# Performance work log

Hardware: AMD Instinct MI355X
Metric: run time of the kernel (lower is better)

Reference implementation:

```python
import jax, jax.numpy as jnp
import numpy as np

# ---- config (mirrors init_kwargs) ----
T = 1024          # num tokens (one causal sequence)
H = 1024          # hidden_size
NQ, NK, D = 16, 4, 64   # q heads, kv heads, head_dim (GQA)
I_DENSE = 4096    # dense FFN intermediate
I_MOE = 512       # expert FFN intermediate
E, K = 8, 2       # num_experts, top_k
EPS = 1e-6
THETA = 10000.0


def setup_inputs() -> dict:
    key = jax.random.key(0)
    ks = jax.random.split(key, 20)
    rn = lambda k, shp: (jax.random.normal(k, shp, dtype=jnp.float32) * 0.02)
    QKV = (NQ + 2 * NK) * D
    return {
        "hidden_states": jax.random.normal(ks[0], (T, H), dtype=jnp.float32),
        "residual": jax.random.normal(ks[1], (T, H), dtype=jnp.float32),
        "positions": jnp.arange(T, dtype=jnp.int32),
        "ln0_w": jnp.ones((H,), jnp.float32),
        "pa0_w": jnp.ones((H,), jnp.float32),
        "ln1_w": jnp.ones((H,), jnp.float32),
        "pa1_w": jnp.ones((H,), jnp.float32),
        # attention weights (stored [in, out] so x @ W)
        "qkv0_w": rn(ks[2], (H, QKV)),
        "o0_w": rn(ks[3], (NQ * D, H)),
        "qkv1_w": rn(ks[4], (H, QKV)),
        "o1_w": rn(ks[5], (NQ * D, H)),
        # dense MLPs (merged gate_up: first half gate, second half up)
        "gu0_w": rn(ks[6], (H, 2 * I_DENSE)),
        "dn0_w": rn(ks[7], (I_DENSE, H)),
        "gu1_w": rn(ks[8], (H, 2 * I_DENSE)),
        "dn1_w": rn(ks[9], (I_DENSE, H)),
        # MoE: router gate + per-expert SwiGLU weights
        "gate_w": rn(ks[10], (H, E)),
        "w13": rn(ks[11], (E, H, 2 * I_MOE)),
        "w2": rn(ks[12], (E, I_MOE, H)),
    }


def _rmsnorm(x, w):
    v = jnp.mean(jnp.square(x.astype(jnp.float32)), axis=-1, keepdims=True)
    return (x.astype(jnp.float32) * jax.lax.rsqrt(v + EPS)).astype(x.dtype) * w


def _add_rmsnorm(x, res, w):
    # sglang fused add + RMSNorm: residual <- x + residual; out <- rmsnorm(residual)
    res = x + res
    return _rmsnorm(res, w), res


def _rope(pos, x):
    # neox-style rotary over full head_dim; x: [T, n_heads, D]
    half = D // 2
    inv_freq = 1.0 / (THETA ** (jnp.arange(half, dtype=jnp.float32) / half))
    f = pos.astype(jnp.float32)[:, None] * inv_freq            # [T, half]
    cos, sin = jnp.cos(f)[:, None, :], jnp.sin(f)[:, None, :]  # [T, 1, half]
    x1, x2 = x[..., :half], x[..., half:]
    return jnp.concatenate([x1 * cos - x2 * sin, x2 * cos + x1 * sin], axis=-1)


def _attention(pos, x, qkv_w, o_w):
    qkv = x @ qkv_w
    q = qkv[:, : NQ * D].reshape(T, NQ, D)
    k = qkv[:, NQ * D : (NQ + NK) * D].reshape(T, NK, D)
    v = qkv[:, (NQ + NK) * D :].reshape(T, NK, D)
    q, k = _rope(pos, q), _rope(pos, k)
    g = NQ // NK
    qg = q.reshape(T, NK, g, D)
    scores = jnp.einsum("tkgd,skd->kgts", qg, k) * (D ** -0.5)  # [NK,g,T,T]
    causal = jnp.tril(jnp.ones((T, T), bool))
    scores = jnp.where(causal, scores, jnp.float32(-1e30))
    p = jax.nn.softmax(scores, axis=-1)
    o = jnp.einsum("kgts,skd->tkgd", p, v).reshape(T, NQ * D)
    return o @ o_w


def _dense_mlp(x, gu_w, dn_w):
    gu = x @ gu_w
    h = jax.nn.silu(gu[:, :I_DENSE]) * gu[:, I_DENSE:]  # SiluAndMul
    return h @ dn_w


def _moe(x, gate_w, w13, w2):
    # router in fp32 (router_dtype == 'float32'), softmax, top-k, no renormalize
    logits = x.astype(jnp.float32) @ gate_w.astype(jnp.float32)  # [T, E]
    probs = jax.nn.softmax(logits, axis=-1)
    topw, topi = jax.lax.top_k(probs, K)                         # [T, K]
    rows = jnp.arange(x.shape[0])[:, None]
    combine = jnp.zeros((x.shape[0], E), jnp.float32).at[rows, topi].set(topw)
    combine = combine.astype(x.dtype)
    out = jnp.zeros_like(x)
    for e in range(E):  # fixed small expert count: grouped-GEMM reference
        g = x @ w13[e]
        h = jax.nn.silu(g[:, :I_MOE]) * g[:, I_MOE:]
        out = out + combine[:, e : e + 1] * (h @ w2[e])
    return out


def reference(hidden_states, residual, positions, ln0_w, pa0_w, ln1_w, pa1_w,
              qkv0_w, o0_w, qkv1_w, o1_w, gu0_w, dn0_w, gu1_w, dn1_w,
              gate_w, w13, w2):
    h, r = _add_rmsnorm(hidden_states, residual, ln0_w)
    h = _attention(positions, h, qkv0_w, o0_w)
    h, r = _add_rmsnorm(h, r, pa0_w)
    shortcut = _moe(h, gate_w, w13, w2)      # MoE runs on the shortcut branch
    h = _dense_mlp(h, gu0_w, dn0_w)
    h, r = _add_rmsnorm(h, r, ln1_w)
    h = _attention(positions, h, qkv1_w, o1_w)
    h, r = _add_rmsnorm(h, r, pa1_w)
    h = _dense_mlp(h, gu1_w, dn1_w)
    h = h + shortcut                          # combine shortcut MoE output
    return h, r
```

## Files before the change

kernel.cpp:

```cpp
#include <hip/hip_runtime.h>
#include <math.h>

namespace {

constexpr int kT = 1024;
constexpr int kH = 1024;
constexpr int kNQ = 16;
constexpr int kNKV = 4;
constexpr int kD = 64;
constexpr int kQKV = (kNQ + 2 * kNKV) * kD;
constexpr int kIDense = 4096;
constexpr int kIMoe = 512;
constexpr int kE = 8;
constexpr float kEps = 1e-6f;
constexpr long kTH = (long)kT * kH;

typedef __attribute__((ext_vector_type(8))) short short8;
typedef __attribute__((ext_vector_type(4))) float f32x4;

__device__ __forceinline__ ushort f2bf(float f) {
    union { float f; uint32_t u; } v; v.f = f;
    uint32_t r = (v.u + 0x7fffu + ((v.u >> 16) & 1u)) >> 16;
    return (ushort)r;
}
__device__ __forceinline__ void gload16(const void* g, void* l) {
    __builtin_amdgcn_global_load_lds(
        (const __attribute__((address_space(1))) void*)g,
        (__attribute__((address_space(3))) void*)l, 16, 0, 0);
}

__global__ __launch_bounds__(256) void add_rmsnorm_kernel(
    const float* __restrict__ xP, int nparts, const float* __restrict__ res,
    const float* __restrict__ w, float* __restrict__ h32,
    ushort* __restrict__ h16, float* __restrict__ r_out)
{
    __shared__ float red[4];
    const int t = blockIdx.x;
    const int i = threadIdx.x;
    const size_t base = (size_t)t * kH;
    float4 s = reinterpret_cast<const float4*>(res + base)[i];
    for (int p = 0; p < nparts; p++) {
        float4 a = reinterpret_cast<const float4*>(xP + p * kTH + base)[i];
        s.x += a.x; s.y += a.y; s.z += a.z; s.w += a.w;
    }
    reinterpret_cast<float4*>(r_out + base)[i] = s;
    float ss = s.x * s.x + s.y * s.y + s.z * s.z + s.w * s.w;
    #pragma unroll
    for (int off = 32; off > 0; off >>= 1) ss += __shfl_down(ss, off);
    if ((i & 63) == 0) red[i >> 6] = ss;
    __syncthreads();
    const float tot = red[0] + red[1] + red[2] + red[3];
    const float inv = rsqrtf(tot * (1.0f / kH) + kEps);
    float4 wv = reinterpret_cast<const float4*>(w)[i];
    float4 o = make_float4(s.x * inv * wv.x, s.y * inv * wv.y,
                           s.z * inv * wv.z, s.w * inv * wv.w);
    reinterpret_cast<float4*>(h32 + base)[i] = o;
    ushort4 u;
    u.x = f2bf(o.x); u.y = f2bf(o.y); u.z = f2bf(o.z); u.w = f2bf(o.w);
    reinterpret_cast<ushort4*>(h16 + base)[i] = u;
}

__global__ __launch_bounds__(256) void transpose_bf16_kernel(
    const float* __restrict__ W, ushort* __restrict__ WT,
    int R, int Cn, int ld_w, long w_z_stride, long wt_z_stride)
{
    __shared__ float tile[64 * 65];
    const int z = blockIdx.z;
    const float* Wz = W + (size_t)z * w_z_stride;
    ushort* WTz = WT + (size_t)z * wt_z_stride;
    const int r0 = blockIdx.y * 64;
    const int c0 = blockIdx.x * 64;
    const int tid = threadIdx.x;
    const int lr = tid >> 4;
    const int lc = (tid & 15) * 4;
    #pragma unroll
    for (int p = 0; p < 4; p++) {
        const int row = p * 16 + lr;
        float4 v = *reinterpret_cast<const float4*>(
            &Wz[(size_t)(r0 + row) * ld_w + c0 + lc]);
        tile[row * 65 + lc + 0] = v.x;
        tile[row * 65 + lc + 1] = v.y;
        tile[row * 65 + lc + 2] = v.z;
        tile[row * 65 + lc + 3] = v.w;
    }
    __syncthreads();
    const int ocl = tid >> 2;
    const int q = tid & 3;
    ushort u[16];
    #pragma unroll
    for (int e = 0; e < 16; e++)
        u[e] = f2bf(tile[(q * 16 + e) * 65 + ocl]);
    ushort* dst = &WTz[(size_t)(c0 + ocl) * R + r0 + q * 16];
    *reinterpret_cast<short8*>(dst) = *reinterpret_cast<short8*>(&u[0]);
    *reinterpret_cast<short8*>(dst + 8) = *reinterpret_cast<short8*>(&u[8]);
}

template <bool GATED>
__global__ __launch_bounds__(256) void mgemm_kernel(
    const ushort* __restrict__ A, const ushort* __restrict__ B,
    float* __restrict__ Cf, ushort* __restrict__ C16,
    const float* __restrict__ scale,
    int lda, int ldb, int ldc, int kc,
    int gate_off_rows, long b_z_stride, int c_z_col, int k_z_off,
    int scale_stride, long c_fstride)
{
    __shared__ __align__(16) ushort As[64 * 64];
    __shared__ __align__(16) ushort Bs[64 * 64];
    __shared__ __align__(16) ushort Us[GATED ? 64 * 64 : 8];

    const int z = blockIdx.z;
    const int gy = gridDim.y;
    const int nf = gridDim.x * gy;
    const int fid = blockIdx.x + gridDim.x * blockIdx.y;
    const int qq = nf >> 3;
    const int id2 = (fid & 7) * qq + (fid >> 3);
    const int m0 = (id2 % gy) * 64;
    const int n0 = (id2 / gy) * 64;

    const int tid = threadIdx.x;
    const ushort* Bz = B + (size_t)z * b_z_stride;
    const int k0 = z * k_z_off;

    const int arow = tid >> 3;
    const int achk = tid & 7;

    const int lane = tid & 63;
    const int wave = tid >> 6;
    const int wr = (wave >> 1) * 32;
    const int wc = (wave & 1) * 32;
    const int lrow = lane & 15;
    const int lg = lane >> 4;

    f32x4 accg[2][2] = {};
    f32x4 accu[2][2] = {};

    for (int kk0 = 0; kk0 < kc; kk0 += 64) {
        const int kbase = k0 + kk0;
        #pragma unroll
        for (int c = 0; c < 2; c++) {
            const int row = c * 32 + arow;
            const int cs = (achk + (row & 7)) & 7;
            gload16(A + (size_t)(m0 + row) * lda + kbase + cs * 8,
                    (char*)As + c * 4096 + tid * 16);
            gload16(Bz + (size_t)(n0 + row) * ldb + kbase + cs * 8,
                    (char*)Bs + c * 4096 + tid * 16);
            if constexpr (GATED)
                gload16(Bz + (size_t)(gate_off_rows + n0 + row) * ldb + kbase + cs * 8,
                        (char*)Us + c * 4096 + tid * 16);
        }
        __syncthreads();

        short8 af[2][2], bfr[2][2];
        #pragma unroll
        for (int mf = 0; mf < 2; mf++)
            #pragma unroll
            for (int kk = 0; kk < 2; kk++) {
                const int r = wr + mf * 16 + lrow;
                const int sl = ((kk * 4 + lg) - (r & 7)) & 7;
                af[mf][kk] = *reinterpret_cast<const short8*>(
                    (const char*)As + r * 128 + sl * 16);
            }
        #pragma unroll
        for (int nf2 = 0; nf2 < 2; nf2++)
            #pragma unroll
            for (int kk = 0; kk < 2; kk++) {
                const int n = wc + nf2 * 16 + lrow;
                const int sl = ((kk * 4 + lg) - (n & 7)) & 7;
                bfr[nf2][kk] = *reinterpret_cast<const short8*>(
                    (const char*)Bs + n * 128 + sl * 16);
            }
        #pragma unroll
        for (int mf = 0; mf < 2; mf++)
            #pragma unroll
            for (int nf2 = 0; nf2 < 2; nf2++)
                #pragma unroll
                for (int kk = 0; kk < 2; kk++)
                    accg[mf][nf2] = __builtin_amdgcn_mfma_f32_16x16x32_bf16(
                        af[mf][kk], bfr[nf2][kk], accg[mf][nf2], 0, 0, 0);
        if constexpr (GATED) {
            short8 uf[2][2];
            #pragma unroll
            for (int nf2 = 0; nf2 < 2; nf2++)
                #pragma unroll
                for (int kk = 0; kk < 2; kk++) {
                    const int n = wc + nf2 * 16 + lrow;
                    const int sl = ((kk * 4 + lg) - (n & 7)) & 7;
                    uf[nf2][kk] = *reinterpret_cast<const short8*>(
                        (const char*)Us + n * 128 + sl * 16);
                }
            #pragma unroll
            for (int mf = 0; mf < 2; mf++)
                #pragma unroll
                for (int nf2 = 0; nf2 < 2; nf2++)
                    #pragma unroll
                    for (int kk = 0; kk < 2; kk++)
                        accu[mf][nf2] = __builtin_amdgcn_mfma_f32_16x16x32_bf16(
                            af[mf][kk], uf[nf2][kk], accu[mf][nf2], 0, 0, 0);
        }
        __syncthreads();
    }

    const int r4 = (lane >> 4) * 4;
    const int cl = lane & 15;
    const int ccol = z * c_z_col;
    float* Cfz = Cf ? Cf + (size_t)z * c_fstride : nullptr;
    #pragma unroll
    for (int mf = 0; mf < 2; mf++) {
        #pragma unroll
        for (int nf2 = 0; nf2 < 2; nf2++) {
            #pragma unroll
            for (int j = 0; j < 4; j++) {
                const int row = m0 + wr + mf * 16 + r4 + j;
                const int col = ccol + n0 + wc + nf2 * 16 + cl;
                if constexpr (GATED) {
                    const float g = accg[mf][nf2][j];
                    const float u = accu[mf][nf2][j];
                    const float sv =
                        scale ? scale[(size_t)row * scale_stride + z] : 1.0f;
                    const float h = (g / (1.0f + __expf(-g))) * u * sv;
                    C16[(size_t)row * ldc + col] = f2bf(h);
                } else {
                    Cfz[(size_t)row * ldc + col] = accg[mf][nf2][j];
                }
            }
        }
    }
}

template <bool GATED>
__global__ __launch_bounds__(512) void mgemm128_kernel(
    const ushort* __restrict__ A, const ushort* __restrict__ B,
    float* __restrict__ Cf, ushort* __restrict__ C16,
    const float* __restrict__ scale,
    int lda, int ldb, int ldc, int kc,
    int gate_off_rows, long b_z_stride, int c_z_col, int k_z_off,
    int scale_stride, long c_fstride)
{
    __shared__ __align__(16) ushort As[64 * 64];
    __shared__ __align__(16) ushort Bs[128 * 64];
    __shared__ __align__(16) ushort Us[GATED ? 128 * 64 : 8];

    const int z = blockIdx.z;
    const int gy = gridDim.y;
    const int nf = gridDim.x * gy;
    const int fid = blockIdx.x + gridDim.x * blockIdx.y;
    const int qq = nf >> 3;
    const int id2 = (fid & 7) * qq + (fid >> 3);
    const int m0 = (id2 % gy) * 64;
    const int n0 = (id2 / gy) * 128;

    const int tid = threadIdx.x;
    const ushort* Bz = B + (size_t)z * b_z_stride;
    const int k0 = z * k_z_off;

    const int sr = tid >> 3;
    const int sc = tid & 7;

    const int lane = tid & 63;
    const int wave = tid >> 6;
    const int wr = (wave >> 2) * 32;
    const int wc = (wave & 3) * 32;
    const int lrow = lane & 15;
    const int lg = lane >> 4;

    f32x4 accg[2][2] = {};
    f32x4 accu[2][2] = {};

    for (int kk0 = 0; kk0 < kc; kk0 += 64) {
        const int kbase = k0 + kk0;
        {
            const int csA = (sc + (sr & 7)) & 7;
            gload16(A + (size_t)(m0 + sr) * lda + kbase + csA * 8,
                    (char*)As + tid * 16);
        }
        #pragma unroll
        for (int c = 0; c < 2; c++) {
            const int row = c * 64 + sr;
            const int cs = (sc + (row & 7)) & 7;
            gload16(Bz + (size_t)(n0 + row) * ldb + kbase + cs * 8,
                    (char*)Bs + c * 8192 + tid * 16);
            if constexpr (GATED)
                gload16(Bz + (size_t)(gate_off_rows + n0 + row) * ldb + kbase + cs * 8,
                        (char*)Us + c * 8192 + tid * 16);
        }
        __syncthreads();

        short8 af[2][2], bfr[2][2];
        #pragma unroll
        for (int mf = 0; mf < 2; mf++)
            #pragma unroll
            for (int kk = 0; kk < 2; kk++) {
                const int r = wr + mf * 16 + lrow;
                const int sl = ((kk * 4 + lg) - (r & 7)) & 7;
                af[mf][kk] = *reinterpret_cast<const short8*>(
                    (const char*)As + r * 128 + sl * 16);
            }
        #pragma unroll
        for (int nf2 = 0; nf2 < 2; nf2++)
            #pragma unroll
            for (int kk = 0; kk < 2; kk++) {
                const int n = wc + nf2 * 16 + lrow;
                const int sl = ((kk * 4 + lg) - (n & 7)) & 7;
                bfr[nf2][kk] = *reinterpret_cast<const short8*>(
                    (const char*)Bs + n * 128 + sl * 16);
            }
        #pragma unroll
        for (int mf = 0; mf < 2; mf++)
            #pragma unroll
            for (int nf2 = 0; nf2 < 2; nf2++)
                #pragma unroll
                for (int kk = 0; kk < 2; kk++)
                    accg[mf][nf2] = __builtin_amdgcn_mfma_f32_16x16x32_bf16(
                        af[mf][kk], bfr[nf2][kk], accg[mf][nf2], 0, 0, 0);
        if constexpr (GATED) {
            short8 uf[2][2];
            #pragma unroll
            for (int nf2 = 0; nf2 < 2; nf2++)
                #pragma unroll
                for (int kk = 0; kk < 2; kk++) {
                    const int n = wc + nf2 * 16 + lrow;
                    const int sl = ((kk * 4 + lg) - (n & 7)) & 7;
                    uf[nf2][kk] = *reinterpret_cast<const short8*>(
                        (const char*)Us + n * 128 + sl * 16);
                }
            #pragma unroll
            for (int mf = 0; mf < 2; mf++)
                #pragma unroll
                for (int nf2 = 0; nf2 < 2; nf2++)
                    #pragma unroll
                    for (int kk = 0; kk < 2; kk++)
                        accu[mf][nf2] = __builtin_amdgcn_mfma_f32_16x16x32_bf16(
                            af[mf][kk], uf[nf2][kk], accu[mf][nf2], 0, 0, 0);
        }
        __syncthreads();
    }

    const int r4 = (lane >> 4) * 4;
    const int cl = lane & 15;
    const int ccol = z * c_z_col;
    float* Cfz = Cf ? Cf + (size_t)z * c_fstride : nullptr;
    #pragma unroll
    for (int mf = 0; mf < 2; mf++) {
        #pragma unroll
        for (int nf2 = 0; nf2 < 2; nf2++) {
            #pragma unroll
            for (int j = 0; j < 4; j++) {
                const int row = m0 + wr + mf * 16 + r4 + j;
                const int col = ccol + n0 + wc + nf2 * 16 + cl;
                if constexpr (GATED) {
                    const float g = accg[mf][nf2][j];
                    const float u = accu[mf][nf2][j];
                    const float sv =
                        scale ? scale[(size_t)row * scale_stride + z] : 1.0f;
                    const float h = (g / (1.0f + __expf(-g))) * u * sv;
                    C16[(size_t)row * ldc + col] = f2bf(h);
                } else {
                    Cfz[(size_t)row * ldc + col] = accg[mf][nf2][j];
                }
            }
        }
    }
}

__global__ __launch_bounds__(256) void rope_pack_kernel(
    const float* __restrict__ qkv, const int* __restrict__ positions,
    ushort* __restrict__ Qb, ushort* __restrict__ Kb)
{
    const int t = blockIdx.x;
    const float pos = (float)positions[t];
    for (int item = threadIdx.x; item < (kNQ + kNKV) * 32; item += 256) {
        const int head = item >> 5;
        const int i = item & 31;
        const float inv_freq = powf(10000.0f, -(float)i * (1.0f / 32.0f));
        const float f = pos * inv_freq;
        float sv, cv;
        sincosf(f, &sv, &cv);
        const size_t off = (size_t)t * kQKV + head * kD;
        const float x1 = qkv[off + i];
        const float x2 = qkv[off + 32 + i];
        const float r1 = x1 * cv - x2 * sv;
        const float r2 = x2 * cv + x1 * sv;
        if (head < kNQ) {
            ushort* q = Qb + ((size_t)head * kT + t) * kD;
            q[i] = f2bf(r1 * 0.125f);
            q[i + 32] = f2bf(r2 * 0.125f);
        } else {
            ushort* k = Kb + ((size_t)(head - kNQ) * kT + t) * kD;
            k[i] = f2bf(r1);
            k[i + 32] = f2bf(r2);
        }
    }
}

__global__ __launch_bounds__(64) void gate_topk_kernel(
    const float* __restrict__ h, const float* __restrict__ gate_w,
    float* __restrict__ combine)
{
    const int t = blockIdx.x;
    const int lane = threadIdx.x;
    float acc[kE] = {};
    for (int i = lane; i < kH; i += 64) {
        const float xv = h[(size_t)t * kH + i];
        const float* gw = gate_w + (size_t)i * kE;
        #pragma unroll
        for (int e = 0; e < kE; e++) acc[e] += xv * gw[e];
    }
    #pragma unroll
    for (int e = 0; e < kE; e++) {
        #pragma unroll
        for (int off = 32; off > 0; off >>= 1) acc[e] += __shfl_down(acc[e], off);
    }
    if (lane == 0) {
        float mx = acc[0];
        #pragma unroll
        for (int e = 1; e < kE; e++) mx = fmaxf(mx, acc[e]);
        float p[kE];
        float s = 0.0f;
        #pragma unroll
        for (int e = 0; e < kE; e++) { p[e] = expf(acc[e] - mx); s += p[e]; }
        const float invs = 1.0f / s;
        #pragma unroll
        for (int e = 0; e < kE; e++) p[e] *= invs;
        int i1 = 0;
        #pragma unroll
        for (int e = 1; e < kE; e++) if (p[e] > p[i1]) i1 = e;
        int i2 = (i1 == 0) ? 1 : 0;
        #pragma unroll
        for (int e = 0; e < kE; e++) if (e != i1 && p[e] > p[i2]) i2 = e;
        float outv[kE];
        #pragma unroll
        for (int e = 0; e < kE; e++) outv[e] = 0.0f;
        outv[i1] = p[i1];
        outv[i2] = p[i2];
        #pragma unroll
        for (int e = 0; e < kE; e++) combine[(size_t)t * kE + e] = outv[e];
    }
}

__global__ __launch_bounds__(256) void attn_mfma_kernel(
    const ushort* __restrict__ Qb, const ushort* __restrict__ Kb,
    const ushort* __restrict__ Vt, float* __restrict__ Opart,
    float* __restrict__ mlpart)
{
    __shared__ __align__(16) ushort Qs[64 * 64];
    __shared__ __align__(16) ushort Ks[64 * 64];
    __shared__ __align__(16) ushort Vs[64 * 64];
    __shared__ __align__(16) ushort Ps[64 * 64];
    const int tid = threadIdx.x;
    const int qbi = (int)gridDim.x - 1 - blockIdx.x;
    const int qb = qbi * 64;
    const int hq = blockIdx.y;
    const int zp = blockIdx.z;
    const int kvh = hq >> 2;

    const int nt = qbi + 1;
    const int halfc = (nt + 1) >> 1;
    const int sbeg = zp ? halfc : 0;
    const int send = zp ? nt : halfc;

    float* Oz = Opart + (((size_t)zp * kNQ + hq) * kT + qb) * kD;
    float* mlz = mlpart + (((size_t)zp * kNQ + hq) * kT + qb) * 2;

    if (sbeg >= send) {
        for (int i = tid; i < 64 * kD; i += 256) Oz[(i >> 6) * kD + (i & 63)] = 0.f;
        for (int i = tid; i < 64; i += 256) { mlz[i * 2] = -1e30f; mlz[i * 2 + 1] = 0.f; }
        return;
    }

    const int lane = tid & 63;
    const int wave = tid >> 6;
    const int lrow = lane & 15;
    const int g = lane >> 4;
    const int srow = tid >> 3;
    const int sx = tid & 7;
    const ushort* Qg = Qb + ((size_t)hq * kT + qb) * kD;
    const ushort* Kg = Kb + (size_t)kvh * kT * kD;
    const ushort* Vg = Vt + (size_t)kvh * kD * kT;
    const int xr = (lrow & 7) << 4;

    #pragma unroll
    for (int c = 0; c < 2; c++) {
        const int row = c * 32 + srow;
        gload16(Qg + (size_t)row * kD + ((sx ^ (row & 7)) * 8),
                (char*)Qs + c * 4096 + tid * 16);
    }
    __syncthreads();
    short8 qf[2];
    #pragma unroll
    for (int kk = 0; kk < 2; kk++)
        qf[kk] = *reinterpret_cast<const short8*>(
            (const char*)Qs + (16 * wave + lrow) * 128 + ((kk * 64 + g * 16) ^ xr));

    f32x4 oacc[4] = {};
    float mrow = -1e30f, lsum = 0.0f;

    for (int ti = sbeg; ti < send; ++ti) {
        const int s0 = ti * 64;
        __syncthreads();
        #pragma unroll
        for (int c = 0; c < 2; c++) {
            const int row = c * 32 + srow;
            gload16(Kg + (size_t)(s0 + row) * kD + ((sx ^ (row & 7)) * 8),
                    (char*)Ks + c * 4096 + tid * 16);
            gload16(Vg + (size_t)row * kT + s0 + ((sx ^ (row & 7)) * 8),
                    (char*)Vs + c * 4096 + tid * 16);
        }
        __syncthreads();

        f32x4 sacc[4] = {};
        #pragma unroll
        for (int nf = 0; nf < 4; nf++) {
            #pragma unroll
            for (int kk = 0; kk < 2; kk++) {
                short8 kf = *reinterpret_cast<const short8*>(
                    (const char*)Ks + (nf * 16 + lrow) * 128 + ((kk * 64 + g * 16) ^ xr));
                sacc[nf] = __builtin_amdgcn_mfma_f32_16x16x32_bf16(
                    kf, qf[kk], sacc[nf], 0, 0, 0);
            }
        }

        const bool diag = (s0 == qb);
        float pv[16];
        float mloc = -1e30f;
        #pragma unroll
        for (int nf = 0; nf < 4; nf++)
            #pragma unroll
            for (int j = 0; j < 4; j++) {
                float s = sacc[nf][j];
                if (diag && (nf * 16 + g * 4 + j > 16 * wave + lrow)) s = -1e30f;
                pv[nf * 4 + j] = s;
                mloc = fmaxf(mloc, s);
            }
        mloc = fmaxf(mloc, __shfl_xor(mloc, 16));
        mloc = fmaxf(mloc, __shfl_xor(mloc, 32));
        const float mnew = fmaxf(mrow, mloc);
        const float alpha = __expf(mrow - mnew);
        float psum = 0.0f;
        #pragma unroll
        for (int j = 0; j < 16; j++) { pv[j] = __expf(pv[j] - mnew); psum += pv[j]; }
        psum += __shfl_xor(psum, 16);
        psum += __shfl_xor(psum, 32);
        lsum = lsum * alpha + psum;
        mrow = mnew;

        const int prow = 16 * wave + lrow;
        #pragma unroll
        for (int nf = 0; nf < 4; nf++)
            #pragma unroll
            for (int jp = 0; jp < 2; jp++) {
                uint32_t pk = (uint32_t)f2bf(pv[nf * 4 + jp * 2]) |
                              ((uint32_t)f2bf(pv[nf * 4 + jp * 2 + 1]) << 16);
                *reinterpret_cast<uint32_t*>(
                    (char*)Ps + prow * 128 + ((nf * 32 + g * 8 + jp * 4) ^ xr)) = pk;
            }

        float aj[4];
        #pragma unroll
        for (int j = 0; j < 4; j++) aj[j] = __shfl(alpha, g * 4 + j);
        #pragma unroll
        for (int nf = 0; nf < 4; nf++)
            #pragma unroll
            for (int j = 0; j < 4; j++) oacc[nf][j] *= aj[j];

        short8 paf[2];
        #pragma unroll
        for (int kk = 0; kk < 2; kk++)
            paf[kk] = *reinterpret_cast<const short8*>(
                (const char*)Ps + prow * 128 + ((kk * 64 + g * 16) ^ xr));
        #pragma unroll
        for (int nf = 0; nf < 4; nf++)
            #pragma unroll
            for (int kk = 0; kk < 2; kk++) {
                short8 vf = *reinterpret_cast<const short8*>(
                    (const char*)Vs + (nf * 16 + lrow) * 128 + ((kk * 64 + g * 16) ^ xr));
                oacc[nf] = __builtin_amdgcn_mfma_f32_16x16x32_bf16(
                    paf[kk], vf, oacc[nf], 0, 0, 0);
            }
    }

    #pragma unroll
    for (int nf = 0; nf < 4; nf++)
        #pragma unroll
        for (int j = 0; j < 4; j++)
            Oz[(16 * wave + g * 4 + j) * kD + nf * 16 + lrow] = oacc[nf][j];
    if (g == 0) {
        mlz[(16 * wave + lrow) * 2 + 0] = mrow;
        mlz[(16 * wave + lrow) * 2 + 1] = lsum;
    }
}

__global__ __launch_bounds__(256) void attn_merge_kernel(
    const float* __restrict__ Opart, const float* __restrict__ mlpart,
    ushort* __restrict__ attn_o)
{
    const int trow = blockIdx.x;
    const int tid = threadIdx.x;
    const int head = tid >> 4;
    const int c4 = (tid & 15) * 4;
    const size_t i0 = ((size_t)head * kT + trow);
    const size_t i1 = (((size_t)kNQ + head) * kT + trow);
    const float m0 = mlpart[i0 * 2], l0 = mlpart[i0 * 2 + 1];
    const float m1 = mlpart[i1 * 2], l1 = mlpart[i1 * 2 + 1];
    const float m = fmaxf(m0, m1);
    const float e0 = __expf(m0 - m), e1 = __expf(m1 - m);
    const float inv = 1.0f / (l0 * e0 + l1 * e1);
    float4 a = *reinterpret_cast<const float4*>(&Opart[i0 * kD + c4]);
    float4 b = *reinterpret_cast<const float4*>(&Opart[i1 * kD + c4]);
    ushort4 u;
    u.x = f2bf((a.x * e0 + b.x * e1) * inv);
    u.y = f2bf((a.y * e0 + b.y * e1) * inv);
    u.z = f2bf((a.z * e0 + b.z * e1) * inv);
    u.w = f2bf((a.w * e0 + b.w * e1) * inv);
    *reinterpret_cast<ushort4*>(
        &attn_o[(size_t)trow * (kNQ * kD) + head * kD + c4]) = u;
}

__global__ __launch_bounds__(256) void final_out_kernel(
    const float* __restrict__ mlpP, const float* __restrict__ scP,
    const float* __restrict__ r, float* __restrict__ out)
{
    const int i = blockIdx.x * 256 + threadIdx.x;
    float4 s = make_float4(0.f, 0.f, 0.f, 0.f);
    #pragma unroll
    for (int p = 0; p < 4; p++) {
        float4 a = reinterpret_cast<const float4*>(mlpP + p * kTH)[i];
        float4 b = reinterpret_cast<const float4*>(scP + p * kTH)[i];
        s.x += a.x + b.x; s.y += a.y + b.y; s.z += a.z + b.z; s.w += a.w + b.w;
    }
    reinterpret_cast<float4*>(out)[i] = s;
    reinterpret_cast<float4*>(out + kTH)[i] =
        reinterpret_cast<const float4*>(r)[i];
}

}

extern "C" void kernel_launch(void* const* d_in, const int* in_sizes, int n_in,
                              void* d_out, int out_size, void* d_ws, size_t ws_size,
                              hipStream_t stream) {
    (void)in_sizes; (void)n_in; (void)out_size; (void)ws_size;
    const float* hidden   = (const float*)d_in[0];
    const float* residual = (const float*)d_in[1];
    const int*   positions= (const int*)d_in[2];
    const float* ln0_w    = (const float*)d_in[3];
    const float* pa0_w    = (const float*)d_in[4];
    const float* ln1_w    = (const float*)d_in[5];
    const float* pa1_w    = (const float*)d_in[6];
    const float* qkv0_w   = (const float*)d_in[7];
    const float* o0_w     = (const float*)d_in[8];
    const float* qkv1_w   = (const float*)d_in[9];
    const float* o1_w     = (const float*)d_in[10];
    const float* gu0_w    = (const float*)d_in[11];
    const float* dn0_w    = (const float*)d_in[12];
    const float* gu1_w    = (const float*)d_in[13];
    const float* dn1_w    = (const float*)d_in[14];
    const float* gate_w   = (const float*)d_in[15];
    const float* w13      = (const float*)d_in[16];
    const float* w2       = (const float*)d_in[17];
    float* out_h = (float*)d_out;

    char* wsb = (char*)d_ws;
    float*  r_buf   = (float*)(wsb + (0ull  << 20));
    float*  h32     = (float*)(wsb + (4ull  << 20));
    float*  t0P     = (float*)(wsb + (8ull  << 20));
    float*  cb_buf  = (float*)(wsb + (8ull  << 20));
    float*  Opart   = (float*)(wsb + (16ull << 20));
    float*  scP     = (float*)(wsb + (24ull << 20));
    ushort* h16     = (ushort*)(wsb + (40ull << 20));
    ushort* ao16    = (ushort*)(wsb + (42ull << 20));
    float*  qkv_buf = (float*)(wsb + (44ull << 20));
    ushort* he16    = (ushort*)(wsb + (44ull << 20));
    float*  ml_buf  = (float*)(wsb + (50ull << 20));
    ushort* wT      = (ushort*)(wsb + (52ull << 20));
    ushort* Qb      = (ushort*)(wsb + (62ull << 20));
    ushort* Kb      = (ushort*)(wsb + (64ull << 20));
    ushort* VtG     = (ushort*)(wsb + (65ull << 20));

    auto transp = [&](const float* W, int R, int Cn, int nz, long zs_in, long zs_out) {
        transpose_bf16_kernel<<<dim3(Cn / 64, R / 64, nz), 256, 0, stream>>>(
            W, wT, R, Cn, Cn, zs_in, zs_out);
    };
    auto attention = [&](const float* qkv_w, const float* o_w) {
        transp(qkv_w, kH, kQKV, 1, 0, 0);
        mgemm_kernel<false><<<dim3(kQKV / 64, kT / 64, 1), 256, 0, stream>>>(
            h16, wT, qkv_buf, nullptr, nullptr, kH, kH, kQKV, kH,
            0, 0, 0, 0, 0, 0);
        rope_pack_kernel<<<kT, 256, 0, stream>>>(qkv_buf, positions, Qb, Kb);
        transpose_bf16_kernel<<<dim3(1, kT / 64, kNKV), 256, 0, stream>>>(
            qkv_buf + (kNQ + kNKV) * kD, VtG, kT, kD, kQKV, kD, (long)kD * kT);
        attn_mfma_kernel<<<dim3(kT / 64, kNQ, 2), 256, 0, stream>>>(
            Qb, Kb, VtG, Opart, ml_buf);
        attn_merge_kernel<<<kT, 256, 0, stream>>>(Opart, ml_buf, ao16);
        transp(o_w, kNQ * kD, kH, 1, 0, 0);
        mgemm_kernel<false><<<dim3(kH / 64, kT / 64, 2), 256, 0, stream>>>(
            ao16, wT, t0P, nullptr, nullptr, kNQ * kD, kNQ * kD, kH, 512,
            0, 0, 0, 512, 0, kTH);
    };
    auto dense_mlp = [&](const float* gu_w, const float* dn_w) {
        transp(gu_w, kH, 2 * kIDense, 1, 0, 0);
        mgemm128_kernel<true><<<dim3(kIDense / 128, kT / 64, 1), 512, 0, stream>>>(
            h16, wT, nullptr, he16, nullptr, kH, kH, kIDense, kH,
            kIDense, 0, 0, 0, 0, 0);
        transp(dn_w, kIDense, kH, 1, 0, 0);
        mgemm128_kernel<false><<<dim3(kH / 128, kT / 64, 4), 512, 0, stream>>>(
            he16, wT, t0P, nullptr, nullptr, kIDense, kIDense, kH, 1024,
            0, 0, 0, 1024, 0, kTH);
    };

    add_rmsnorm_kernel<<<kT, 256, 0, stream>>>(hidden, 1, residual, ln0_w, h32, h16, r_buf);
    attention(qkv0_w, o0_w);
    add_rmsnorm_kernel<<<kT, 256, 0, stream>>>(t0P, 2, r_buf, pa0_w, h32, h16, r_buf);
    gate_topk_kernel<<<kT, 64, 0, stream>>>(h32, gate_w, cb_buf);
    transp(w13, kH, 2 * kIMoe, kE, (long)kH * 2 * kIMoe, (long)kH * 2 * kIMoe);
    mgemm128_kernel<true><<<dim3(kIMoe / 128, kT / 64, kE), 512, 0, stream>>>(
        h16, wT, nullptr, he16, cb_buf, kH, kH, kIDense, kH,
        kIMoe, (long)kH * 2 * kIMoe, kIMoe, 0, kE, 0);
    transp(w2, kE * kIMoe, kH, 1, 0, 0);
    mgemm128_kernel<false><<<dim3(kH / 128, kT / 64, 4), 512, 0, stream>>>(
        he16, wT, scP, nullptr, nullptr, kIDense, kIDense, kH, 1024,
        0, 0, 0, 1024, 0, kTH);
    dense_mlp(gu0_w, dn0_w);
    add_rmsnorm_kernel<<<kT, 256, 0, stream>>>(t0P, 4, r_buf, ln1_w, h32, h16, r_buf);
    attention(qkv1_w, o1_w);
    add_rmsnorm_kernel<<<kT, 256, 0, stream>>>(t0P, 2, r_buf, pa1_w, h32, h16, r_buf);
    dense_mlp(gu1_w, dn1_w);
    final_out_kernel<<<(kT * kH / 4) / 256, 256, 0, stream>>>(t0P, scP, r_buf, out_h);
}
```

Measured before the change: 321.9 us.

## Route MoE tokens sparsely to top-k experts instead of dense all-expert GEMMs

```diff
diff --git a/kernel.cpp b/kernel.cpp
--- a/kernel.cpp
+++ b/kernel.cpp
@@ -22,6 +22,10 @@
     union { float f; uint32_t u; } v; v.f = f;
     uint32_t r = (v.u + 0x7fffu + ((v.u >> 16) & 1u)) >> 16;
     return (ushort)r;
+}
+__device__ __forceinline__ float bf2f(ushort b) {
+    union { uint32_t u; float f; } v; v.u = ((uint32_t)b) << 16;
+    return v.f;
 }
 __device__ __forceinline__ void gload16(const void* g, void* l) {
     __builtin_amdgcn_global_load_lds(
@@ -360,6 +364,229 @@
             }
         }
     }
+}
+
+__global__ __launch_bounds__(512) void moe_w13_kernel(
+    const ushort* __restrict__ Ah, const ushort* __restrict__ w13T,
+    ushort* __restrict__ heC, const float* __restrict__ combine,
+    const int* __restrict__ counts, const int* __restrict__ idx)
+{
+    __shared__ __align__(16) ushort As[64 * 64];
+    __shared__ __align__(16) ushort Bs[128 * 64];
+    __shared__ __align__(16) ushort Us[128 * 64];
+
+    const int e = blockIdx.z;
+    const int cnt = counts[e];
+    const int gy = gridDim.y;
+    const int nf = gridDim.x * gy;
+    const int fid = blockIdx.x + gridDim.x * blockIdx.y;
+    const int qq = nf >> 3;
+    const int id2 = (fid & 7) * qq + (fid >> 3);
+    const int m0 = (id2 % gy) * 64;
+    const int n0 = (id2 / gy) * 128;
+    if (m0 >= cnt) return;
+
+    const ushort* Bz = w13T + (size_t)e * (2 * kIMoe) * kH;
+    const int* idxe = idx + e * kT;
+    const int tid = threadIdx.x;
+    const int sr = tid >> 3;
+    const int sc = tid & 7;
+    const int lane = tid & 63;
+    const int wave = tid >> 6;
+    const int wr = (wave >> 2) * 32;
+    const int wc = (wave & 3) * 32;
+    const int lrow = lane & 15;
+    const int lg = lane >> 4;
+
+    int gA = m0 + sr;
+    const int tokA = idxe[gA < cnt ? gA : cnt - 1];
+
+    f32x4 accg[2][2] = {};
+    f32x4 accu[2][2] = {};
+
+    for (int kk0 = 0; kk0 < kH; kk0 += 64) {
+        {
+            const int csA = (sc + (sr & 7)) & 7;
+            gload16(Ah + (size_t)tokA * kH + kk0 + csA * 8, (char*)As + tid * 16);
+        }
+        #pragma unroll
+        for (int c = 0; c < 2; c++) {
+            const int row = c * 64 + sr;
+            const int cs = (sc + (row & 7)) & 7;
+            gload16(Bz + (size_t)(n0 + row) * kH + kk0 + cs * 8,
+                    (char*)Bs + c * 8192 + tid * 16);
+            gload16(Bz + (size_t)(kIMoe + n0 + row) * kH + kk0 + cs * 8,
+                    (char*)Us + c * 8192 + tid * 16);
+        }
+        __syncthreads();
+
+        short8 af[2][2], bfr[2][2], uf[2][2];
+        #pragma unroll
+        for (int mf = 0; mf < 2; mf++)
+            #pragma unroll
+            for (int kk = 0; kk < 2; kk++) {
+                const int r = wr + mf * 16 + lrow;
+                const int sl = ((kk * 4 + lg) - (r & 7)) & 7;
+                af[mf][kk] = *reinterpret_cast<const short8*>(
+                    (const char*)As + r * 128 + sl * 16);
+            }
+        #pragma unroll
+        for (int nf2 = 0; nf2 < 2; nf2++)
+            #pragma unroll
+            for (int kk = 0; kk < 2; kk++) {
+                const int n = wc + nf2 * 16 + lrow;
+                const int sl = ((kk * 4 + lg) - (n & 7)) & 7;
+                bfr[nf2][kk] = *reinterpret_cast<const short8*>(
+                    (const char*)Bs + n * 128 + sl * 16);
+                uf[nf2][kk] = *reinterpret_cast<const short8*>(
+                    (const char*)Us + n * 128 + sl * 16);
+            }
+        #pragma unroll
+        for (int mf = 0; mf < 2; mf++)
+            #pragma unroll
+            for (int nf2 = 0; nf2 < 2; nf2++)
+                #pragma unroll
+                for (int kk = 0; kk < 2; kk++) {
+                    accg[mf][nf2] = __builtin_amdgcn_mfma_f32_16x16x32_bf16(
+                        af[mf][kk], bfr[nf2][kk], accg[mf][nf2], 0, 0, 0);
+                    accu[mf][nf2] = __builtin_amdgcn_mfma_f32_16x16x32_bf16(
+                        af[mf][kk], uf[nf2][kk], accu[mf][nf2], 0, 0, 0);
+                }
+        __syncthreads();
+    }
+
+    const int r4 = (lane >> 4) * 4;
+    const int cl = lane & 15;
+    #pragma unroll
+    for (int mf = 0; mf < 2; mf++) {
+        #pragma unroll
+        for (int nf2 = 0; nf2 < 2; nf2++) {
+            #pragma unroll
+            for (int j = 0; j < 4; j++) {
+                const int gl = m0 + wr + mf * 16 + r4 + j;
+                if (gl < cnt) {
+                    const int token = idxe[gl];
+                    const float sv = combine[(size_t)token * kE + e];
+                    const float g = accg[mf][nf2][j];
+                    const float u = accu[mf][nf2][j];
+                    const float h = (g / (1.0f + __expf(-g))) * u * sv;
+                    heC[((size_t)e * kT + gl) * kIMoe + n0 + wc + nf2 * 16 + cl] =
+                        f2bf(h);
+                }
+            }
+        }
+    }
+}
+
+__global__ __launch_bounds__(512) void moe_w2_kernel(
+    const ushort* __restrict__ heC, const ushort* __restrict__ w2T,
+    ushort* __restrict__ Osp, const int* __restrict__ counts)
+{
+    __shared__ __align__(16) ushort As[64 * 64];
+    __shared__ __align__(16) ushort Bs[128 * 64];
+
+    const int e = blockIdx.z;
+    const int cnt = counts[e];
+    const int gy = gridDim.y;
+    const int nf = gridDim.x * gy;
+    const int fid = blockIdx.x + gridDim.x * blockIdx.y;
+    const int qq = nf >> 3;
+    const int id2 = (fid & 7) * qq + (fid >> 3);
+    const int m0 = (id2 % gy) * 64;
+    const int n0 = (id2 / gy) * 128;
+    if (m0 >= cnt) return;
+
+    const ushort* Az = heC + (size_t)e * kT * kIMoe;
+    const ushort* Bz = w2T + (size_t)e * kIMoe;
+    const int tid = threadIdx.x;
+    const int sr = tid >> 3;
+    const int sc = tid & 7;
+    const int lane = tid & 63;
+    const int wave = tid >> 6;
+    const int wr = (wave >> 2) * 32;
+    const int wc = (wave & 3) * 32;
+    const int lrow = lane & 15;
+    const int lg = lane >> 4;
+
+    f32x4 acc[2][2] = {};
+
+    for (int kk0 = 0; kk0 < kIMoe; kk0 += 64) {
+        {
+            const int csA = (sc + (sr & 7)) & 7;
+            gload16(Az + (size_t)(m0 + sr) * kIMoe + kk0 + csA * 8,
+                    (char*)As + tid * 16);
+        }
+        #pragma unroll
+        for (int c = 0; c < 2; c++) {
+            const int row = c * 64 + sr;
+            const int cs = (sc + (row & 7)) & 7;
+            gload16(Bz + (size_t)(n0 + row) * kIDense + kk0 + cs * 8,
+                    (char*)Bs + c * 8192 + tid * 16);
+        }
+        __syncthreads();
+
+        short8 af[2][2], bfr[2][2];
+        #pragma unroll
+        for (int mf = 0; mf < 2; mf++)
+            #pragma unroll
+            for (int kk = 0; kk < 2; kk++) {
+                const int r = wr + mf * 16 + lrow;
+                const int sl = ((kk * 4 + lg) - (r & 7)) & 7;
+                af[mf][kk] = *reinterpret_cast<const short8*>(
+                    (const char*)As + r * 128 + sl * 16);
+            }
+        #pragma unroll
+        for (int nf2 = 0; nf2 < 2; nf2++)
+            #pragma unroll
+            for (int kk = 0; kk < 2; kk++) {
+                const int n = wc + nf2 * 16 + lrow;
+                const int sl = ((kk * 4 + lg) - (n & 7)) & 7;
+                bfr[nf2][kk] = *reinterpret_cast<const short8*>(
+                    (const char*)Bs + n * 128 + sl * 16);
+            }
+        #pragma unroll
+        for (int mf = 0; mf < 2; mf++)
+            #pragma unroll
+            for (int nf2 = 0; nf2 < 2; nf2++)
+                #pragma unroll
+                for (int kk = 0; kk < 2; kk++)
+                    acc[mf][nf2] = __builtin_amdgcn_mfma_f32_16x16x32_bf16(
+                        af[mf][kk], bfr[nf2][kk], acc[mf][nf2], 0, 0, 0);
+        __syncthreads();
+    }
+
+    const int r4 = (lane >> 4) * 4;
+    const int cl = lane & 15;
+    #pragma unroll
+    for (int mf = 0; mf < 2; mf++) {
+        #pragma unroll
+        for (int nf2 = 0; nf2 < 2; nf2++) {
+            #pragma unroll
+            for (int j = 0; j < 4; j++) {
+                const int gl = m0 + wr + mf * 16 + r4 + j;
+                if (gl < cnt)
+                    Osp[((size_t)e * kT + gl) * kH + n0 + wc + nf2 * 16 + cl] =
+                        f2bf(acc[mf][nf2][j]);
+            }
+        }
+    }
+}
+
+__global__ __launch_bounds__(256) void moe_combine_kernel(
+    const ushort* __restrict__ Osp, const int* __restrict__ slotmap,
+    float* __restrict__ sc)
+{
+    const int t = blockIdx.x;
+    const int c4 = threadIdx.x * 4;
+    const int s0 = slotmap[t * 2 + 0];
+    const int s1 = slotmap[t * 2 + 1];
+    const ushort* p0 = Osp + ((size_t)(s0 >> 16) * kT + (s0 & 0xffff)) * kH + c4;
+    const ushort* p1 = Osp + ((size_t)(s1 >> 16) * kT + (s1 & 0xffff)) * kH + c4;
+    ushort4 a = *reinterpret_cast<const ushort4*>(p0);
+    ushort4 b = *reinterpret_cast<const ushort4*>(p1);
+    float4 o = make_float4(bf2f(a.x) + bf2f(b.x), bf2f(a.y) + bf2f(b.y),
+                           bf2f(a.z) + bf2f(b.z), bf2f(a.w) + bf2f(b.w));
+    *reinterpret_cast<float4*>(&sc[(size_t)t * kH + c4]) = o;
 }
 
 __global__ __launch_bounds__(256) void rope_pack_kernel(
@@ -394,7 +621,8 @@
 
 __global__ __launch_bounds__(64) void gate_topk_kernel(
     const float* __restrict__ h, const float* __restrict__ gate_w,
-    float* __restrict__ combine)
+    float* __restrict__ combine, int* __restrict__ counts,
+    int* __restrict__ idx, int* __restrict__ slotmap)
 {
     const int t = blockIdx.x;
     const int lane = threadIdx.x;
@@ -434,6 +662,12 @@
         outv[i2] = p[i2];
         #pragma unroll
         for (int e = 0; e < kE; e++) combine[(size_t)t * kE + e] = outv[e];
+        const int s1 = atomicAdd(&counts[i1], 1);
+        idx[i1 * kT + s1] = t;
+        slotmap[t * 2 + 0] = (i1 << 16) | s1;
+        const int s2 = atomicAdd(&counts[i2], 1);
+        idx[i2 * kT + s2] = t;
+        slotmap[t * 2 + 1] = (i2 << 16) | s2;
     }
 }
 
@@ -616,16 +850,15 @@
 }
 
 __global__ __launch_bounds__(256) void final_out_kernel(
-    const float* __restrict__ mlpP, const float* __restrict__ scP,
+    const float* __restrict__ mlpP, const float* __restrict__ sc,
     const float* __restrict__ r, float* __restrict__ out)
 {
     const int i = blockIdx.x * 256 + threadIdx.x;
-    float4 s = make_float4(0.f, 0.f, 0.f, 0.f);
+    float4 s = reinterpret_cast<const float4*>(sc)[i];
     #pragma unroll
     for (int p = 0; p < 4; p++) {
         float4 a = reinterpret_cast<const float4*>(mlpP + p * kTH)[i];
-        float4 b = reinterpret_cast<const float4*>(scP + p * kTH)[i];
-        s.x += a.x + b.x; s.y += a.y + b.y; s.z += a.z + b.z; s.w += a.w + b.w;
+        s.x += a.x; s.y += a.y; s.z += a.z; s.w += a.w;
     }
     reinterpret_cast<float4*>(out)[i] = s;
     reinterpret_cast<float4*>(out + kTH)[i] =
@@ -663,17 +896,21 @@
     float*  h32     = (float*)(wsb + (4ull  << 20));
     float*  t0P     = (float*)(wsb + (8ull  << 20));
     float*  cb_buf  = (float*)(wsb + (8ull  << 20));
+    int*    cnt_buf = (int*)  (wsb + (8ull  << 20) + (1 << 15));
+    int*    idx_buf = (int*)  (wsb + (8ull  << 20) + (1 << 16));
+    int*    slot_buf= (int*)  (wsb + (8ull  << 20) + (1 << 17));
     float*  Opart   = (float*)(wsb + (16ull << 20));
-    float*  scP     = (float*)(wsb + (24ull << 20));
-    ushort* h16     = (ushort*)(wsb + (40ull << 20));
-    ushort* ao16    = (ushort*)(wsb + (42ull << 20));
-    float*  qkv_buf = (float*)(wsb + (44ull << 20));
-    ushort* he16    = (ushort*)(wsb + (44ull << 20));
-    float*  ml_buf  = (float*)(wsb + (50ull << 20));
-    ushort* wT      = (ushort*)(wsb + (52ull << 20));
-    ushort* Qb      = (ushort*)(wsb + (62ull << 20));
-    ushort* Kb      = (ushort*)(wsb + (64ull << 20));
-    ushort* VtG     = (ushort*)(wsb + (65ull << 20));
+    float*  sc_buf  = (float*)(wsb + (24ull << 20));
+    ushort* Osp     = (ushort*)(wsb + (28ull << 20));
+    ushort* h16     = (ushort*)(wsb + (44ull << 20));
+    ushort* ao16    = (ushort*)(wsb + (46ull << 20));
+    float*  qkv_buf = (float*)(wsb + (48ull << 20));
+    ushort* he16    = (ushort*)(wsb + (48ull << 20));
+    float*  ml_buf  = (float*)(wsb + (54ull << 20));
+    ushort* wT      = (ushort*)(wsb + (56ull << 20));
+    ushort* Qb      = (ushort*)(wsb + (66ull << 20));
+    ushort* Kb      = (ushort*)(wsb + (68ull << 20));
+    ushort* VtG     = (ushort*)(wsb + (69ull << 20));
 
     auto transp = [&](const float* W, int R, int Cn, int nz, long zs_in, long zs_out) {
         transpose_bf16_kernel<<<dim3(Cn / 64, R / 64, nz), 256, 0, stream>>>(
@@ -709,19 +946,20 @@
     add_rmsnorm_kernel<<<kT, 256, 0, stream>>>(hidden, 1, residual, ln0_w, h32, h16, r_buf);
     attention(qkv0_w, o0_w);
     add_rmsnorm_kernel<<<kT, 256, 0, stream>>>(t0P, 2, r_buf, pa0_w, h32, h16, r_buf);
-    gate_topk_kernel<<<kT, 64, 0, stream>>>(h32, gate_w, cb_buf);
+    hipMemsetAsync(cnt_buf, 0, kE * sizeof(int), stream);
+    gate_topk_kernel<<<kT, 64, 0, stream>>>(h32, gate_w, cb_buf, cnt_buf,
+                                            idx_buf, slot_buf);
     transp(w13, kH, 2 * kIMoe, kE, (long)kH * 2 * kIMoe, (long)kH * 2 * kIMoe);
-    mgemm128_kernel<true><<<dim3(kIMoe / 128, kT / 64, kE), 512, 0, stream>>>(
-        h16, wT, nullptr, he16, cb_buf, kH, kH, kIDense, kH,
-        kIMoe, (long)kH * 2 * kIMoe, kIMoe, 0, kE, 0);
+    moe_w13_kernel<<<dim3(kIMoe / 128, kT / 64, kE), 512, 0, stream>>>(
+        h16, wT, he16, cb_buf, cnt_buf, idx_buf);
     transp(w2, kE * kIMoe, kH, 1, 0, 0);
-    mgemm128_kernel<false><<<dim3(kH / 128, kT / 64, 4), 512, 0, stream>>>(
-        he16, wT, scP, nullptr, nullptr, kIDense, kIDense, kH, 1024,
-        0, 0, 0, 1024, 0, kTH);
+    moe_w2_kernel<<<dim3(kH / 128, kT / 64, kE), 512, 0, stream>>>(
+        he16, wT, Osp, cnt_buf);
+    moe_combine_kernel<<<kT, 256, 0, stream>>>(Osp, slot_buf, sc_buf);
     dense_mlp(gu0_w, dn0_w);
     add_rmsnorm_kernel<<<kT, 256, 0, stream>>>(t0P, 4, r_buf, ln1_w, h32, h16, r_buf);
     attention(qkv1_w, o1_w);
     add_rmsnorm_kernel<<<kT, 256, 0, stream>>>(t0P, 2, r_buf, pa1_w, h32, h16, r_buf);
     dense_mlp(gu1_w, dn1_w);
-    final_out_kernel<<<(kT * kH / 4) / 256, 256, 0, stream>>>(t0P, scP, r_buf, out_h);
-}
+    final_out_kernel<<<(kT * kH / 4) / 256, 256, 0, stream>>>(t0P, sc_buf, r_buf, out_h);
+}
```

New measurement: 338.7 us. 1.05x slower.
